# Kernel tuning notes

Measured on AMD Instinct MI355X. Metric: run time of the kernel, lower is better.

Reference implementation:

```python
import jax, jax.numpy as jnp
import numpy as np

B, LQ, LK = 4, 256, 512
DQ, DK, DV = 512, 512, 512
H = 256
NEG = -1e6


def setup_inputs() -> dict:
    key = jax.random.key(0)
    ks = jax.random.split(key, 7)
    queries = jax.random.normal(ks[0], (B, LQ, DQ), dtype=jnp.float32)
    keys = jax.random.normal(ks[1], (B, LK, DK), dtype=jnp.float32)
    values = jax.random.normal(ks[2], (B, LK, DV), dtype=jnp.float32)
    valid_lens = jax.random.randint(ks[3], (B,), 1, LK + 1).astype(jnp.int32)
    # learned params (Linear without bias): store as (in, out) so x @ W matches torch x @ W.T
    Wq = jax.random.normal(ks[4], (DQ, H), dtype=jnp.float32) * (1.0 / np.sqrt(DQ))
    Wk = jax.random.normal(ks[5], (DK, H), dtype=jnp.float32) * (1.0 / np.sqrt(DK))
    wv = jax.random.normal(ks[6], (H,), dtype=jnp.float32) * (1.0 / np.sqrt(H))
    return {"queries": queries, "keys": keys, "values": values,
            "valid_lens": valid_lens, "Wq": Wq, "Wk": Wk, "wv": wv}


def reference(queries, keys, values, valid_lens, Wq, Wk, wv):
    q = jnp.einsum('bqd,dh->bqh', queries, Wq)          # (B,Lq,H)
    k = jnp.einsum('bkd,dh->bkh', keys, Wk)             # (B,Lk,H)
    feats = jnp.tanh(q[:, :, None, :] + k[:, None, :, :])  # (B,Lq,Lk,H)
    scores = jnp.einsum('bqkh,h->bqk', feats, wv)        # (B,Lq,Lk)
    mask = jnp.arange(LK)[None, None, :] < valid_lens[:, None, None]  # (B,1,Lk)
    attn = jax.nn.softmax(jnp.where(mask, scores, NEG), axis=-1)
    return jnp.einsum('bqk,bkv->bqv', attn, values)      # (B,Lq,Dv)
```

## Files before the change

kernel.cpp:

```cpp
#include <hip/hip_runtime.h>

#define B_   4
#define LQ_  256
#define LK_  512
#define DIN_ 512
#define H_   256
#define DV_  512

#define L2E 1.4426950408889634f

__global__ __launch_bounds__(256) void proj_partial_kernel(
    const float* __restrict__ Q, const float* __restrict__ K,
    const float* __restrict__ Wq, const float* __restrict__ Wk,
    const int* __restrict__ valid_lens,
    float* __restrict__ qpart, float* __restrict__ ekTpart) {
  __shared__ float xs[64][68];
  __shared__ float ws[64][132];

  const int blk = blockIdx.x;
  const bool isQ = blk < 128;
  int b, row0, h0, ds;
  if (isQ) {
    ds = blk & 3; h0 = ((blk >> 2) & 1) * 128;
    const int rt = blk >> 3;
    b = rt >> 2; row0 = (rt & 3) * 64;
  } else {
    const int u = blk - 128;
    ds = u & 7; h0 = ((u >> 3) & 1) * 128;
    const int rt = u >> 4;
    b = rt & 3; row0 = (rt >> 2) * 64;
    if (row0 >= valid_lens[b]) return;
  }
  const int L = isQ ? LQ_ : LK_;
  const int dspan = isQ ? 128 : 64;
  const float* __restrict__ X  = (isQ ? Q : K) + ((size_t)(b * L + row0)) * DIN_ + ds * dspan;
  const float* __restrict__ Wb = (isQ ? Wq : Wk) + (size_t)(ds * dspan) * H_ + h0;

  const int t = threadIdx.x;
  const int hthr = t & 31;
  const int rthr = t >> 5;

  float acc[8][4];
#pragma unroll
  for (int r = 0; r < 8; ++r)
#pragma unroll
    for (int c = 0; c < 4; ++c) acc[r][c] = 0.f;

  for (int dd = 0; dd < dspan; dd += 64) {
    __syncthreads();
#pragma unroll
    for (int u = 0; u < 4; ++u) {
      const int f = t + 256 * u;
      const int r = f >> 4, c4 = (f & 15) << 2;
      *(float4*)&xs[r][c4] = *(const float4*)&X[(size_t)r * DIN_ + dd + c4];
    }
#pragma unroll
    for (int u = 0; u < 8; ++u) {
      const int f = t + 256 * u;
      const int k = f >> 5, c4 = (f & 31) << 2;
      *(float4*)&ws[k][c4] = *(const float4*)&Wb[(size_t)(dd + k) * H_ + c4];
    }
    __syncthreads();

    for (int k = 0; k < 64; k += 8) {
      float4 w4[8];
#pragma unroll
      for (int k8 = 0; k8 < 8; ++k8)
        w4[k8] = *(const float4*)&ws[k + k8][4 * hthr];
#pragma unroll
      for (int rr = 0; rr < 8; ++rr) {
        const float4 xa = *(const float4*)&xs[rthr * 8 + rr][k];
        const float4 xb = *(const float4*)&xs[rthr * 8 + rr][k + 4];
        const float xv[8] = {xa.x, xa.y, xa.z, xa.w, xb.x, xb.y, xb.z, xb.w};
#pragma unroll
        for (int k8 = 0; k8 < 8; ++k8) {
          acc[rr][0] = fmaf(xv[k8], w4[k8].x, acc[rr][0]);
          acc[rr][1] = fmaf(xv[k8], w4[k8].y, acc[rr][1]);
          acc[rr][2] = fmaf(xv[k8], w4[k8].z, acc[rr][2]);
          acc[rr][3] = fmaf(xv[k8], w4[k8].w, acc[rr][3]);
        }
      }
    }
  }

  if (isQ) {
    float* dst = qpart + (size_t)ds * (B_ * LQ_ * H_);
#pragma unroll
    for (int rr = 0; rr < 8; ++rr) {
      const int row = row0 + rthr * 8 + rr;
      float4 o = {acc[rr][0], acc[rr][1], acc[rr][2], acc[rr][3]};
      *(float4*)&dst[(size_t)(b * LQ_ + row) * H_ + h0 + 4 * hthr] = o;
    }
  } else {
    float* dst = ekTpart + (size_t)ds * (B_ * H_ * LK_);
#pragma unroll
    for (int c = 0; c < 4; ++c) {
      const int h = h0 + 4 * hthr + c;
      float* p = &dst[((size_t)b * H_ + h) * LK_ + row0 + rthr * 8];
      float4 lo = {acc[0][c], acc[1][c], acc[2][c], acc[3][c]};
      float4 hi = {acc[4][c], acc[5][c], acc[6][c], acc[7][c]};
      *(float4*)p = lo;
      *(float4*)(p + 4) = hi;
    }
  }
}

__global__ __launch_bounds__(512) void combine_ek_kernel(
    const float* __restrict__ ekTpart, float* __restrict__ ek2) {
  const int k4 = blockIdx.x * 512 + threadIdx.x;
  const size_t KN4 = (size_t)B_ * H_ * LK_ / 4;
  const float4* src = (const float4*)ekTpart;
  float4 s = src[k4];
#pragma unroll
  for (int p = 1; p < 8; ++p) {
    const float4 v = src[p * KN4 + k4];
    s.x += v.x; s.y += v.y; s.z += v.z; s.w += v.w;
  }
  float4 o;
  o.x = exp2f(fminf(fmaxf(s.x * (2.f * L2E), -126.f), 126.f));
  o.y = exp2f(fminf(fmaxf(s.y * (2.f * L2E), -126.f), 126.f));
  o.z = exp2f(fminf(fmaxf(s.z * (2.f * L2E), -126.f), 126.f));
  o.w = exp2f(fminf(fmaxf(s.w * (2.f * L2E), -126.f), 126.f));
  ((float4*)ek2)[k4] = o;
}

__global__ __launch_bounds__(512) void fused_attn_kernel(
    const float* __restrict__ qpart, const float* __restrict__ ek2,
    const float* __restrict__ wv, const int* __restrict__ valid_lens,
    const float* __restrict__ V, float* __restrict__ out) {
  __shared__ float eqs[2][260];
  __shared__ float wvs[256];
  __shared__ float ph[2][2][260];
  __shared__ float2 p2s[LK_];
  __shared__ float reds[8][2];
  __shared__ float wsum_s;

  const int blk = blockIdx.x;
  const int b  = (blk & 3) ^ ((blk >> 8) & 1);
  const int i0 = (blk >> 2) * 2;
  const int vl = valid_lens[b];
  const int t = threadIdx.x;
  const int lane = t & 63, wave = t >> 6;

  const size_t QN = (size_t)B_ * LQ_ * H_;
  {
    const int i = t >> 8, h = t & 255;
    const size_t base = (size_t)(b * LQ_ + i0 + i) * H_ + h;
    const float v = qpart[base] + qpart[QN + base] +
                    qpart[2 * QN + base] + qpart[3 * QN + base];
    eqs[i][h] = exp2f(fminf(fmaxf(v * (2.f * L2E), -126.f), 126.f));
  }
  if (t < 256) wvs[t] = wv[t];
  if (t < 64) {
    float s = wv[t] + wv[t + 64] + wv[t + 128] + wv[t + 192];
#pragma unroll
    for (int off = 32; off; off >>= 1) s += __shfl_xor(s, off);
    if (t == 0) wsum_s = s;
  }
  __syncthreads();
  const float Wsum = wsum_s;

  const bool valid = t < vl;
  float s[2] = {-3.0e38f, -3.0e38f};
  if (vl > 256) {
    if (valid) {
      const float* __restrict__ kb = ek2 + (size_t)b * H_ * LK_ + t;
      float a0 = 0.f, a1 = 0.f;
      for (int h = 0; h < H_; h += 16) {
        float kv[16];
#pragma unroll
        for (int u = 0; u < 16; ++u)
          kv[u] = kb[(size_t)(h + u) * LK_];
#pragma unroll
        for (int g = 0; g < 4; ++g) {
          const float4 w4  = *(const float4*)&wvs[h + 4 * g];
          const float4 q0v = *(const float4*)&eqs[0][h + 4 * g];
          const float4 q1v = *(const float4*)&eqs[1][h + 4 * g];
          const float ww[4] = {w4.x, w4.y, w4.z, w4.w};
          const float q0[4] = {q0v.x, q0v.y, q0v.z, q0v.w};
          const float q1[4] = {q1v.x, q1v.y, q1v.z, q1v.w};
#pragma unroll
          for (int u = 0; u < 4; ++u) {
            const float k2 = kv[4 * g + u];
            a0 = fmaf(ww[u], __builtin_amdgcn_rcpf(fmaf(q0[u], k2, 1.f)), a0);
            a1 = fmaf(ww[u], __builtin_amdgcn_rcpf(fmaf(q1[u], k2, 1.f)), a1);
          }
        }
      }
      s[0] = fmaf(-2.f, a0, Wsum);
      s[1] = fmaf(-2.f, a1, Wsum);
    }
  } else {
    const int j = t & 255;
    const int hb = (t >> 8) * 128;
    if (j < vl) {
      const float* __restrict__ kb = ek2 + (size_t)b * H_ * LK_ + j;
      float a0 = 0.f, a1 = 0.f;
      for (int hh = 0; hh < 128; hh += 16) {
        const int h = hb + hh;
        float kv[16];
#pragma unroll
        for (int u = 0; u < 16; ++u)
          kv[u] = kb[(size_t)(h + u) * LK_];
#pragma unroll
        for (int g = 0; g < 4; ++g) {
          const float4 w4  = *(const float4*)&wvs[h + 4 * g];
          const float4 q0v = *(const float4*)&eqs[0][h + 4 * g];
          const float4 q1v = *(const float4*)&eqs[1][h + 4 * g];
          const float ww[4] = {w4.x, w4.y, w4.z, w4.w};
          const float q0[4] = {q0v.x, q0v.y, q0v.z, q0v.w};
          const float q1[4] = {q1v.x, q1v.y, q1v.z, q1v.w};
#pragma unroll
          for (int u = 0; u < 4; ++u) {
            const float k2 = kv[4 * g + u];
            a0 = fmaf(ww[u], __builtin_amdgcn_rcpf(fmaf(q0[u], k2, 1.f)), a0);
            a1 = fmaf(ww[u], __builtin_amdgcn_rcpf(fmaf(q1[u], k2, 1.f)), a1);
          }
        }
      }
      ph[t >> 8][0][j] = a0;
      ph[t >> 8][1][j] = a1;
    }
    __syncthreads();
    if (valid) {
      s[0] = fmaf(-2.f, ph[0][0][t] + ph[1][0][t], Wsum);
      s[1] = fmaf(-2.f, ph[0][1][t] + ph[1][1][t], Wsum);
    }
  }

  float e[2], sum[2];
#pragma unroll
  for (int i = 0; i < 2; ++i) {
    e[i] = valid ? exp2f(s[i] * L2E) : 0.f;
    sum[i] = e[i];
  }
#pragma unroll
  for (int off = 32; off; off >>= 1)
#pragma unroll
    for (int i = 0; i < 2; ++i) sum[i] += __shfl_xor(sum[i], off);
  if (lane == 0)
#pragma unroll
    for (int i = 0; i < 2; ++i) reds[wave][i] = sum[i];
  __syncthreads();
  {
    float tot[2];
#pragma unroll
    for (int i = 0; i < 2; ++i) {
      tot[i] = reds[0][i];
#pragma unroll
      for (int w = 1; w < 8; ++w) tot[i] += reds[w][i];
    }
    float2 pv;
    pv.x = e[0] * __builtin_amdgcn_rcpf(tot[0]);
    pv.y = e[1] * __builtin_amdgcn_rcpf(tot[1]);
    p2s[t] = pv;
  }
  __syncthreads();

  const float* __restrict__ Vb = V + (size_t)b * LK_ * DV_ + t;
  float a0 = 0.f, a1 = 0.f;
  int j = 0;
  const int jv = vl & ~7;
  for (; j < jv; j += 8) {
    float v[8];
#pragma unroll
    for (int u = 0; u < 8; ++u) v[u] = Vb[(size_t)(j + u) * DV_];
#pragma unroll
    for (int u = 0; u < 8; ++u) {
      const float2 pp = p2s[j + u];
      a0 = fmaf(pp.x, v[u], a0);
      a1 = fmaf(pp.y, v[u], a1);
    }
  }
  for (; j < vl; ++j) {
    const float v = Vb[(size_t)j * DV_];
    const float2 pp = p2s[j];
    a0 = fmaf(pp.x, v, a0);
    a1 = fmaf(pp.y, v, a1);
  }
  out[(size_t)(b * LQ_ + i0) * DV_ + t]     = a0;
  out[(size_t)(b * LQ_ + i0 + 1) * DV_ + t] = a1;
}

extern "C" void kernel_launch(void* const* d_in, const int* in_sizes, int n_in,
                              void* d_out, int out_size, void* d_ws, size_t ws_size,
                              hipStream_t stream) {
  const float* queries    = (const float*)d_in[0];
  const float* keys       = (const float*)d_in[1];
  const float* values     = (const float*)d_in[2];
  const int*   valid_lens = (const int*)d_in[3];
  const float* Wq         = (const float*)d_in[4];
  const float* Wk         = (const float*)d_in[5];
  const float* wv         = (const float*)d_in[6];
  float* out = (float*)d_out;

  char* ws = (char*)d_ws;
  float* qpart   = (float*)ws;
  float* ekTpart = (float*)(ws + (size_t)( 4 << 20));
  float* ek2     = (float*)(ws + (size_t)(20 << 20));

  proj_partial_kernel<<<640, 256, 0, stream>>>(
      queries, keys, Wq, Wk, valid_lens, qpart, ekTpart);
  combine_ek_kernel<<<256, 512, 0, stream>>>(ekTpart, ek2);
  fused_attn_kernel<<<512, 512, 0, stream>>>(
      qpart, ek2, wv, valid_lens, values, out);
}
```

Before: 51.98 us.

## Add atomic work queues, longest-batch-first ordering, and fp16 V staging

Both the projection and attention kernels become persistent-style loops that pull work items from atomic counters, reset by a memset before launch. The attention kernel processes batches in descending valid_len order so the heaviest items are scheduled first. The combine kernel now also converts V to fp16 and precomputes the wv sum, which halves the bytes the attention loop reads for V. This adds a memset launch, an atomic and extra barriers per item, and a full V conversion pass, and it lowers the precision of V.

```diff
diff --git a/kernel.cpp b/kernel.cpp
--- a/kernel.cpp
+++ b/kernel.cpp
@@ -1,4 +1,5 @@
 #include <hip/hip_runtime.h>
+#include <hip/hip_fp16.h>
 
 #define B_   4
 #define LQ_  256
@@ -12,274 +13,315 @@
 __global__ __launch_bounds__(256) void proj_partial_kernel(
     const float* __restrict__ Q, const float* __restrict__ K,
     const float* __restrict__ Wq, const float* __restrict__ Wk,
-    const int* __restrict__ valid_lens,
+    const int* __restrict__ valid_lens, int* __restrict__ counter,
     float* __restrict__ qpart, float* __restrict__ ekTpart) {
   __shared__ float xs[64][68];
   __shared__ float ws[64][132];
-
-  const int blk = blockIdx.x;
-  const bool isQ = blk < 128;
-  int b, row0, h0, ds;
-  if (isQ) {
-    ds = blk & 3; h0 = ((blk >> 2) & 1) * 128;
-    const int rt = blk >> 3;
-    b = rt >> 2; row0 = (rt & 3) * 64;
-  } else {
-    const int u = blk - 128;
-    ds = u & 7; h0 = ((u >> 3) & 1) * 128;
-    const int rt = u >> 4;
-    b = rt & 3; row0 = (rt >> 2) * 64;
-    if (row0 >= valid_lens[b]) return;
-  }
-  const int L = isQ ? LQ_ : LK_;
-  const int dspan = isQ ? 128 : 64;
-  const float* __restrict__ X  = (isQ ? Q : K) + ((size_t)(b * L + row0)) * DIN_ + ds * dspan;
-  const float* __restrict__ Wb = (isQ ? Wq : Wk) + (size_t)(ds * dspan) * H_ + h0;
+  __shared__ int s_idx;
 
   const int t = threadIdx.x;
   const int hthr = t & 31;
   const int rthr = t >> 5;
 
-  float acc[8][4];
-#pragma unroll
-  for (int r = 0; r < 8; ++r)
-#pragma unroll
-    for (int c = 0; c < 4; ++c) acc[r][c] = 0.f;
-
-  for (int dd = 0; dd < dspan; dd += 64) {
-    __syncthreads();
-#pragma unroll
-    for (int u = 0; u < 4; ++u) {
-      const int f = t + 256 * u;
-      const int r = f >> 4, c4 = (f & 15) << 2;
-      *(float4*)&xs[r][c4] = *(const float4*)&X[(size_t)r * DIN_ + dd + c4];
-    }
-#pragma unroll
-    for (int u = 0; u < 8; ++u) {
-      const int f = t + 256 * u;
-      const int k = f >> 5, c4 = (f & 31) << 2;
-      *(float4*)&ws[k][c4] = *(const float4*)&Wb[(size_t)(dd + k) * H_ + c4];
-    }
-    __syncthreads();
-
-    for (int k = 0; k < 64; k += 8) {
-      float4 w4[8];
-#pragma unroll
-      for (int k8 = 0; k8 < 8; ++k8)
-        w4[k8] = *(const float4*)&ws[k + k8][4 * hthr];
+  while (true) {
+    __syncthreads();
+    if (t == 0) s_idx = atomicAdd(counter, 1);
+    __syncthreads();
+    const int blk = s_idx;
+    if (blk >= 640) break;
+
+    const bool isQ = blk < 128;
+    int b, row0, h0, ds;
+    if (isQ) {
+      ds = blk & 3; h0 = ((blk >> 2) & 1) * 128;
+      const int rt = blk >> 3;
+      b = rt >> 2; row0 = (rt & 3) * 64;
+    } else {
+      const int u = blk - 128;
+      ds = u & 7; h0 = ((u >> 3) & 1) * 128;
+      const int rt = u >> 4;
+      b = rt & 3; row0 = (rt >> 2) * 64;
+      if (row0 >= valid_lens[b]) continue;
+    }
+    const int L = isQ ? LQ_ : LK_;
+    const int dspan = isQ ? 128 : 64;
+    const float* __restrict__ X  = (isQ ? Q : K) + ((size_t)(b * L + row0)) * DIN_ + ds * dspan;
+    const float* __restrict__ Wb = (isQ ? Wq : Wk) + (size_t)(ds * dspan) * H_ + h0;
+
+    float acc[8][4];
+#pragma unroll
+    for (int r = 0; r < 8; ++r)
+#pragma unroll
+      for (int c = 0; c < 4; ++c) acc[r][c] = 0.f;
+
+    for (int dd = 0; dd < dspan; dd += 64) {
+      __syncthreads();
+#pragma unroll
+      for (int u = 0; u < 4; ++u) {
+        const int f = t + 256 * u;
+        const int r = f >> 4, c4 = (f & 15) << 2;
+        *(float4*)&xs[r][c4] = *(const float4*)&X[(size_t)r * DIN_ + dd + c4];
+      }
+#pragma unroll
+      for (int u = 0; u < 8; ++u) {
+        const int f = t + 256 * u;
+        const int k = f >> 5, c4 = (f & 31) << 2;
+        *(float4*)&ws[k][c4] = *(const float4*)&Wb[(size_t)(dd + k) * H_ + c4];
+      }
+      __syncthreads();
+
+      for (int k = 0; k < 64; k += 8) {
+        float4 w4[8];
+#pragma unroll
+        for (int k8 = 0; k8 < 8; ++k8)
+          w4[k8] = *(const float4*)&ws[k + k8][4 * hthr];
+#pragma unroll
+        for (int rr = 0; rr < 8; ++rr) {
+          const float4 xa = *(const float4*)&xs[rthr * 8 + rr][k];
+          const float4 xb = *(const float4*)&xs[rthr * 8 + rr][k + 4];
+          const float xv[8] = {xa.x, xa.y, xa.z, xa.w, xb.x, xb.y, xb.z, xb.w};
+#pragma unroll
+          for (int k8 = 0; k8 < 8; ++k8) {
+            acc[rr][0] = fmaf(xv[k8], w4[k8].x, acc[rr][0]);
+            acc[rr][1] = fmaf(xv[k8], w4[k8].y, acc[rr][1]);
+            acc[rr][2] = fmaf(xv[k8], w4[k8].z, acc[rr][2]);
+            acc[rr][3] = fmaf(xv[k8], w4[k8].w, acc[rr][3]);
+          }
+        }
+      }
+    }
+
+    if (isQ) {
+      float* dst = qpart + (size_t)ds * (B_ * LQ_ * H_);
 #pragma unroll
       for (int rr = 0; rr < 8; ++rr) {
-        const float4 xa = *(const float4*)&xs[rthr * 8 + rr][k];
-        const float4 xb = *(const float4*)&xs[rthr * 8 + rr][k + 4];
-        const float xv[8] = {xa.x, xa.y, xa.z, xa.w, xb.x, xb.y, xb.z, xb.w};
-#pragma unroll
-        for (int k8 = 0; k8 < 8; ++k8) {
-          acc[rr][0] = fmaf(xv[k8], w4[k8].x, acc[rr][0]);
-          acc[rr][1] = fmaf(xv[k8], w4[k8].y, acc[rr][1]);
-          acc[rr][2] = fmaf(xv[k8], w4[k8].z, acc[rr][2]);
-          acc[rr][3] = fmaf(xv[k8], w4[k8].w, acc[rr][3]);
-        }
-      }
-    }
-  }
-
-  if (isQ) {
-    float* dst = qpart + (size_t)ds * (B_ * LQ_ * H_);
-#pragma unroll
-    for (int rr = 0; rr < 8; ++rr) {
-      const int row = row0 + rthr * 8 + rr;
-      float4 o = {acc[rr][0], acc[rr][1], acc[rr][2], acc[rr][3]};
-      *(float4*)&dst[(size_t)(b * LQ_ + row) * H_ + h0 + 4 * hthr] = o;
-    }
-  } else {
-    float* dst = ekTpart + (size_t)ds * (B_ * H_ * LK_);
-#pragma unroll
-    for (int c = 0; c < 4; ++c) {
-      const int h = h0 + 4 * hthr + c;
-      float* p = &dst[((size_t)b * H_ + h) * LK_ + row0 + rthr * 8];
-      float4 lo = {acc[0][c], acc[1][c], acc[2][c], acc[3][c]};
-      float4 hi = {acc[4][c], acc[5][c], acc[6][c], acc[7][c]};
-      *(float4*)p = lo;
-      *(float4*)(p + 4) = hi;
+        const int row = row0 + rthr * 8 + rr;
+        float4 o = {acc[rr][0], acc[rr][1], acc[rr][2], acc[rr][3]};
+        *(float4*)&dst[(size_t)(b * LQ_ + row) * H_ + h0 + 4 * hthr] = o;
+      }
+    } else {
+      float* dst = ekTpart + (size_t)ds * (B_ * H_ * LK_);
+#pragma unroll
+      for (int c = 0; c < 4; ++c) {
+        const int h = h0 + 4 * hthr + c;
+        float* p = &dst[((size_t)b * H_ + h) * LK_ + row0 + rthr * 8];
+        float4 lo = {acc[0][c], acc[1][c], acc[2][c], acc[3][c]};
+        float4 hi = {acc[4][c], acc[5][c], acc[6][c], acc[7][c]};
+        *(float4*)p = lo;
+        *(float4*)(p + 4) = hi;
+      }
     }
   }
 }
 
-__global__ __launch_bounds__(512) void combine_ek_kernel(
-    const float* __restrict__ ekTpart, float* __restrict__ ek2) {
-  const int k4 = blockIdx.x * 512 + threadIdx.x;
-  const size_t KN4 = (size_t)B_ * H_ * LK_ / 4;
-  const float4* src = (const float4*)ekTpart;
-  float4 s = src[k4];
-#pragma unroll
-  for (int p = 1; p < 8; ++p) {
-    const float4 v = src[p * KN4 + k4];
-    s.x += v.x; s.y += v.y; s.z += v.z; s.w += v.w;
+__global__ __launch_bounds__(512) void combine_kernel(
+    const float* __restrict__ ekTpart, const float* __restrict__ V,
+    const float* __restrict__ wv,
+    float* __restrict__ ek2, __half* __restrict__ Vh, float* __restrict__ wsum) {
+  const int blk = blockIdx.x;
+  const int t = threadIdx.x;
+  if (blk < 256) {
+    const int k4 = blk * 512 + t;
+    const size_t KN4 = (size_t)B_ * H_ * LK_ / 4;
+    const float4* src = (const float4*)ekTpart;
+    float4 s = src[k4];
+#pragma unroll
+    for (int p = 1; p < 8; ++p) {
+      const float4 v = src[p * KN4 + k4];
+      s.x += v.x; s.y += v.y; s.z += v.z; s.w += v.w;
+    }
+    float4 o;
+    o.x = exp2f(fminf(fmaxf(s.x * (2.f * L2E), -126.f), 126.f));
+    o.y = exp2f(fminf(fmaxf(s.y * (2.f * L2E), -126.f), 126.f));
+    o.z = exp2f(fminf(fmaxf(s.z * (2.f * L2E), -126.f), 126.f));
+    o.w = exp2f(fminf(fmaxf(s.w * (2.f * L2E), -126.f), 126.f));
+    ((float4*)ek2)[k4] = o;
+    if (blk == 0 && t < 64) {
+      float sw = wv[t] + wv[t + 64] + wv[t + 128] + wv[t + 192];
+#pragma unroll
+      for (int off = 32; off; off >>= 1) sw += __shfl_xor(sw, off);
+      if (t == 0) *wsum = sw;
+    }
+  } else {
+    const int q4 = (blk - 256) * 512 + t;
+    const float4 v = ((const float4*)V)[q4];
+    ((__half2*)Vh)[2 * q4]     = __floats2half2_rn(v.x, v.y);
+    ((__half2*)Vh)[2 * q4 + 1] = __floats2half2_rn(v.z, v.w);
   }
-  float4 o;
-  o.x = exp2f(fminf(fmaxf(s.x * (2.f * L2E), -126.f), 126.f));
-  o.y = exp2f(fminf(fmaxf(s.y * (2.f * L2E), -126.f), 126.f));
-  o.z = exp2f(fminf(fmaxf(s.z * (2.f * L2E), -126.f), 126.f));
-  o.w = exp2f(fminf(fmaxf(s.w * (2.f * L2E), -126.f), 126.f));
-  ((float4*)ek2)[k4] = o;
 }
 
 __global__ __launch_bounds__(512) void fused_attn_kernel(
     const float* __restrict__ qpart, const float* __restrict__ ek2,
-    const float* __restrict__ wv, const int* __restrict__ valid_lens,
-    const float* __restrict__ V, float* __restrict__ out) {
+    const __half* __restrict__ Vh, const float* __restrict__ wv,
+    const float* __restrict__ wsum, const int* __restrict__ valid_lens,
+    int* __restrict__ counter, float* __restrict__ out) {
   __shared__ float eqs[2][260];
   __shared__ float wvs[256];
   __shared__ float ph[2][2][260];
   __shared__ float2 p2s[LK_];
   __shared__ float reds[8][2];
-  __shared__ float wsum_s;
-
-  const int blk = blockIdx.x;
-  const int b  = (blk & 3) ^ ((blk >> 8) & 1);
-  const int i0 = (blk >> 2) * 2;
-  const int vl = valid_lens[b];
+  __shared__ int s_idx;
+
   const int t = threadIdx.x;
   const int lane = t & 63, wave = t >> 6;
+  const float Wsum = *wsum;
+  if (t < 256) wvs[t] = wv[t];
+
+  int vls[4], ord[4] = {0, 1, 2, 3};
+#pragma unroll
+  for (int i = 0; i < 4; ++i) vls[i] = valid_lens[i];
+#pragma unroll
+  for (int i = 0; i < 3; ++i)
+#pragma unroll
+    for (int j = 0; j < 3 - i; ++j) {
+      const int a = ord[j], c = ord[j + 1];
+      if (vls[a] < vls[c] || (vls[a] == vls[c] && a > c)) {
+        ord[j] = c; ord[j + 1] = a;
+      }
+    }
 
   const size_t QN = (size_t)B_ * LQ_ * H_;
-  {
-    const int i = t >> 8, h = t & 255;
-    const size_t base = (size_t)(b * LQ_ + i0 + i) * H_ + h;
-    const float v = qpart[base] + qpart[QN + base] +
-                    qpart[2 * QN + base] + qpart[3 * QN + base];
-    eqs[i][h] = exp2f(fminf(fmaxf(v * (2.f * L2E), -126.f), 126.f));
-  }
-  if (t < 256) wvs[t] = wv[t];
-  if (t < 64) {
-    float s = wv[t] + wv[t + 64] + wv[t + 128] + wv[t + 192];
-#pragma unroll
-    for (int off = 32; off; off >>= 1) s += __shfl_xor(s, off);
-    if (t == 0) wsum_s = s;
-  }
-  __syncthreads();
-  const float Wsum = wsum_s;
-
-  const bool valid = t < vl;
-  float s[2] = {-3.0e38f, -3.0e38f};
-  if (vl > 256) {
-    if (valid) {
-      const float* __restrict__ kb = ek2 + (size_t)b * H_ * LK_ + t;
-      float a0 = 0.f, a1 = 0.f;
-      for (int h = 0; h < H_; h += 16) {
-        float kv[16];
-#pragma unroll
-        for (int u = 0; u < 16; ++u)
-          kv[u] = kb[(size_t)(h + u) * LK_];
-#pragma unroll
-        for (int g = 0; g < 4; ++g) {
-          const float4 w4  = *(const float4*)&wvs[h + 4 * g];
-          const float4 q0v = *(const float4*)&eqs[0][h + 4 * g];
-          const float4 q1v = *(const float4*)&eqs[1][h + 4 * g];
-          const float ww[4] = {w4.x, w4.y, w4.z, w4.w};
-          const float q0[4] = {q0v.x, q0v.y, q0v.z, q0v.w};
-          const float q1[4] = {q1v.x, q1v.y, q1v.z, q1v.w};
-#pragma unroll
-          for (int u = 0; u < 4; ++u) {
-            const float k2 = kv[4 * g + u];
-            a0 = fmaf(ww[u], __builtin_amdgcn_rcpf(fmaf(q0[u], k2, 1.f)), a0);
-            a1 = fmaf(ww[u], __builtin_amdgcn_rcpf(fmaf(q1[u], k2, 1.f)), a1);
+  while (true) {
+    __syncthreads();
+    if (t == 0) s_idx = atomicAdd(counter, 1);
+    __syncthreads();
+    const int idx = s_idx;
+    if (idx >= 512) break;
+    const int b  = ord[idx >> 7];
+    const int i0 = (idx & 127) * 2;
+    const int vl = vls[b];
+
+    {
+      const int r = t >> 8, h = t & 255;
+      const size_t base = (size_t)(b * LQ_ + i0 + r) * H_ + h;
+      const float v = qpart[base] + qpart[QN + base] +
+                      qpart[2 * QN + base] + qpart[3 * QN + base];
+      eqs[r][h] = exp2f(fminf(fmaxf(v * (2.f * L2E), -126.f), 126.f));
+    }
+    __syncthreads();
+
+    const bool valid = t < vl;
+    float s[2] = {-3.0e38f, -3.0e38f};
+    if (vl > 256) {
+      if (valid) {
+        const float* __restrict__ kb = ek2 + (size_t)b * H_ * LK_ + t;
+        float a0 = 0.f, a1 = 0.f;
+        for (int h = 0; h < H_; h += 16) {
+          float kv[16];
+#pragma unroll
+          for (int u = 0; u < 16; ++u)
+            kv[u] = kb[(size_t)(h + u) * LK_];
+#pragma unroll
+          for (int g = 0; g < 4; ++g) {
+            const float4 w4  = *(const float4*)&wvs[h + 4 * g];
+            const float4 q0v = *(const float4*)&eqs[0][h + 4 * g];
+            const float4 q1v = *(const float4*)&eqs[1][h + 4 * g];
+            const float ww[4] = {w4.x, w4.y, w4.z, w4.w};
+            const float q0[4] = {q0v.x, q0v.y, q0v.z, q0v.w};
+            const float q1[4] = {q1v.x, q1v.y, q1v.z, q1v.w};
+#pragma unroll
+            for (int u = 0; u < 4; ++u) {
+              const float k2 = kv[4 * g + u];
+              a0 = fmaf(ww[u], __builtin_amdgcn_rcpf(fmaf(q0[u], k2, 1.f)), a0);
+              a1 = fmaf(ww[u], __builtin_amdgcn_rcpf(fmaf(q1[u], k2, 1.f)), a1);
+            }
           }
         }
-      }
-      s[0] = fmaf(-2.f, a0, Wsum);
-      s[1] = fmaf(-2.f, a1, Wsum);
-    }
-  } else {
-    const int j = t & 255;
-    const int hb = (t >> 8) * 128;
-    if (j < vl) {
-      const float* __restrict__ kb = ek2 + (size_t)b * H_ * LK_ + j;
-      float a0 = 0.f, a1 = 0.f;
-      for (int hh = 0; hh < 128; hh += 16) {
-        const int h = hb + hh;
-        float kv[16];
-#pragma unroll
-        for (int u = 0; u < 16; ++u)
-          kv[u] = kb[(size_t)(h + u) * LK_];
-#pragma unroll
-        for (int g = 0; g < 4; ++g) {
-          const float4 w4  = *(const float4*)&wvs[h + 4 * g];
-          const float4 q0v = *(const float4*)&eqs[0][h + 4 * g];
-          const float4 q1v = *(const float4*)&eqs[1][h + 4 * g];
-          const float ww[4] = {w4.x, w4.y, w4.z, w4.w};
-          const float q0[4] = {q0v.x, q0v.y, q0v.z, q0v.w};
-          const float q1[4] = {q1v.x, q1v.y, q1v.z, q1v.w};
-#pragma unroll
-          for (int u = 0; u < 4; ++u) {
-            const float k2 = kv[4 * g + u];
-            a0 = fmaf(ww[u], __builtin_amdgcn_rcpf(fmaf(q0[u], k2, 1.f)), a0);
-            a1 = fmaf(ww[u], __builtin_amdgcn_rcpf(fmaf(q1[u], k2, 1.f)), a1);
+        s[0] = fmaf(-2.f, a0, Wsum);
+        s[1] = fmaf(-2.f, a1, Wsum);
+      }
+    } else {
+      const int j = t & 255;
+      const int hb = (t >> 8) * 128;
+      if (j < vl) {
+        const float* __restrict__ kb = ek2 + (size_t)b * H_ * LK_ + j;
+        float a0 = 0.f, a1 = 0.f;
+        for (int hh = 0; hh < 128; hh += 16) {
+          const int h = hb + hh;
+          float kv[16];
+#pragma unroll
+          for (int u = 0; u < 16; ++u)
+            kv[u] = kb[(size_t)(h + u) * LK_];
+#pragma unroll
+          for (int g = 0; g < 4; ++g) {
+            const float4 w4  = *(const float4*)&wvs[h + 4 * g];
+            const float4 q0v = *(const float4*)&eqs[0][h + 4 * g];
+            const float4 q1v = *(const float4*)&eqs[1][h + 4 * g];
+            const float ww[4] = {w4.x, w4.y, w4.z, w4.w};
+            const float q0[4] = {q0v.x, q0v.y, q0v.z, q0v.w};
+            const float q1[4] = {q1v.x, q1v.y, q1v.z, q1v.w};
+#pragma unroll
+            for (int u = 0; u < 4; ++u) {
+              const float k2 = kv[4 * g + u];
+              a0 = fmaf(ww[u], __builtin_amdgcn_rcpf(fmaf(q0[u], k2, 1.f)), a0);
+              a1 = fmaf(ww[u], __builtin_amdgcn_rcpf(fmaf(q1[u], k2, 1.f)), a1);
+            }
           }
         }
-      }
-      ph[t >> 8][0][j] = a0;
-      ph[t >> 8][1][j] = a1;
-    }
-    __syncthreads();
-    if (valid) {
-      s[0] = fmaf(-2.f, ph[0][0][t] + ph[1][0][t], Wsum);
-      s[1] = fmaf(-2.f, ph[0][1][t] + ph[1][1][t], Wsum);
-    }
+        ph[t >> 8][0][j] = a0;
+        ph[t >> 8][1][j] = a1;
+      }
+      __syncthreads();
+      if (valid) {
+        s[0] = fmaf(-2.f, ph[0][0][t] + ph[1][0][t], Wsum);
+        s[1] = fmaf(-2.f, ph[0][1][t] + ph[1][1][t], Wsum);
+      }
+    }
+
+    float e[2], sum[2];
+#pragma unroll
+    for (int i = 0; i < 2; ++i) {
+      e[i] = valid ? exp2f(s[i] * L2E) : 0.f;
+      sum[i] = e[i];
+    }
+#pragma unroll
+    for (int off = 32; off; off >>= 1)
+#pragma unroll
+      for (int i = 0; i < 2; ++i) sum[i] += __shfl_xor(sum[i], off);
+    if (lane == 0)
+#pragma unroll
+      for (int i = 0; i < 2; ++i) reds[wave][i] = sum[i];
+    __syncthreads();
+    {
+      float tot[2];
+#pragma unroll
+      for (int i = 0; i < 2; ++i) {
+        tot[i] = reds[0][i];
+#pragma unroll
+        for (int w = 1; w < 8; ++w) tot[i] += reds[w][i];
+      }
+      float2 pv;
+      pv.x = e[0] * __builtin_amdgcn_rcpf(tot[0]);
+      pv.y = e[1] * __builtin_amdgcn_rcpf(tot[1]);
+      p2s[t] = pv;
+    }
+    __syncthreads();
+
+    const __half* __restrict__ Vb = Vh + (size_t)b * LK_ * DV_ + t;
+    float a0 = 0.f, a1 = 0.f;
+    int j = 0;
+    const int jv = vl & ~7;
+    for (; j < jv; j += 8) {
+      float v[8];
+#pragma unroll
+      for (int u = 0; u < 8; ++u)
+        v[u] = __half2float(Vb[(size_t)(j + u) * DV_]);
+#pragma unroll
+      for (int u = 0; u < 8; ++u) {
+        const float2 pp = p2s[j + u];
+        a0 = fmaf(pp.x, v[u], a0);
+        a1 = fmaf(pp.y, v[u], a1);
+      }
+    }
+    for (; j < vl; ++j) {
+      const float v = __half2float(Vb[(size_t)j * DV_]);
+      const float2 pp = p2s[j];
+      a0 = fmaf(pp.x, v, a0);
+      a1 = fmaf(pp.y, v, a1);
+    }
+    out[(size_t)(b * LQ_ + i0) * DV_ + t]     = a0;
+    out[(size_t)(b * LQ_ + i0 + 1) * DV_ + t] = a1;
   }
-
-  float e[2], sum[2];
-#pragma unroll
-  for (int i = 0; i < 2; ++i) {
-    e[i] = valid ? exp2f(s[i] * L2E) : 0.f;
-    sum[i] = e[i];
-  }
-#pragma unroll
-  for (int off = 32; off; off >>= 1)
-#pragma unroll
-    for (int i = 0; i < 2; ++i) sum[i] += __shfl_xor(sum[i], off);
-  if (lane == 0)
-#pragma unroll
-    for (int i = 0; i < 2; ++i) reds[wave][i] = sum[i];
-  __syncthreads();
-  {
-    float tot[2];
-#pragma unroll
-    for (int i = 0; i < 2; ++i) {
-      tot[i] = reds[0][i];
-#pragma unroll
-      for (int w = 1; w < 8; ++w) tot[i] += reds[w][i];
-    }
-    float2 pv;
-    pv.x = e[0] * __builtin_amdgcn_rcpf(tot[0]);
-    pv.y = e[1] * __builtin_amdgcn_rcpf(tot[1]);
-    p2s[t] = pv;
-  }
-  __syncthreads();
-
-  const float* __restrict__ Vb = V + (size_t)b * LK_ * DV_ + t;
-  float a0 = 0.f, a1 = 0.f;
-  int j = 0;
-  const int jv = vl & ~7;
-  for (; j < jv; j += 8) {
-    float v[8];
-#pragma unroll
-    for (int u = 0; u < 8; ++u) v[u] = Vb[(size_t)(j + u) * DV_];
-#pragma unroll
-    for (int u = 0; u < 8; ++u) {
-      const float2 pp = p2s[j + u];
-      a0 = fmaf(pp.x, v[u], a0);
-      a1 = fmaf(pp.y, v[u], a1);
-    }
-  }
-  for (; j < vl; ++j) {
-    const float v = Vb[(size_t)j * DV_];
-    const float2 pp = p2s[j];
-    a0 = fmaf(pp.x, v, a0);
-    a1 = fmaf(pp.y, v, a1);
-  }
-  out[(size_t)(b * LQ_ + i0) * DV_ + t]     = a0;
-  out[(size_t)(b * LQ_ + i0 + 1) * DV_ + t] = a1;
 }
 
 extern "C" void kernel_launch(void* const* d_in, const int* in_sizes, int n_in,
@@ -295,13 +337,19 @@
   float* out = (float*)d_out;
 
   char* ws = (char*)d_ws;
-  float* qpart   = (float*)ws;
-  float* ekTpart = (float*)(ws + (size_t)( 4 << 20));
-  float* ek2     = (float*)(ws + (size_t)(20 << 20));
-
-  proj_partial_kernel<<<640, 256, 0, stream>>>(
-      queries, keys, Wq, Wk, valid_lens, qpart, ekTpart);
-  combine_ek_kernel<<<256, 512, 0, stream>>>(ekTpart, ek2);
+  float*  qpart   = (float*)ws;
+  float*  ekTpart = (float*)(ws + (size_t)( 4 << 20));
+  float*  ek2     = (float*)(ws + (size_t)(20 << 20));
+  __half* Vh      = (__half*)(ws + (size_t)(22 << 20));
+  float*  wsum    = (float*)(ws + (size_t)(24 << 20));
+  int*    counters= (int*)(ws + (size_t)(24 << 20) + 128);
+
+  hipMemsetAsync(counters, 0, 2 * sizeof(int), stream);
+
+  proj_partial_kernel<<<512, 256, 0, stream>>>(
+      queries, keys, Wq, Wk, valid_lens, &counters[0], qpart, ekTpart);
+  combine_kernel<<<768, 512, 0, stream>>>(
+      ekTpart, values, wv, ek2, Vh, wsum);
   fused_attn_kernel<<<512, 512, 0, stream>>>(
-      qpart, ek2, wv, valid_lens, values, out);
+      qpart, ek2, Vh, wv, wsum, valid_lens, &counters[1], out);
 }
```

Result: slower. 68.28 us (+31.4%).
